# Kernel tuning notes

Measured on AMD Instinct MI355X. Metric: run time of the kernel, lower is better.

Reference implementation:

```python
import jax, jax.numpy as jnp
import numpy as np

N_HEADS = 8
EPS = 1e-8


def _build_gp_map():
    # Cl(4,1) geometric-product structure constants. Blade index = 5-bit mask,
    # e1..e5 = bits 0..4; metric (+,+,+,+,-): e5 (bit 4) squares to -1.
    def pc(n):
        return bin(n).count("1")
    g = np.zeros((32, 32, 32), np.float32)
    for a in range(32):
        for b in range(32):
            swaps = 0
            aa = a >> 1
            while aa:
                swaps += pc(aa & b)
                aa >>= 1
            sign = -1.0 if (swaps & 1) else 1.0
            if (a & b) & 0b10000:  # shared e5 factor contributes -1
                sign = -sign
            g[a, b, a ^ b] = sign
    return g

GP_MAP = jnp.asarray(_build_gp_map())          # (32,32,32)
BIVEC_IDX = jnp.array([3, 5, 6, 9, 10, 12, 17, 18, 20, 24])  # grade-2 blades
SCALAR_VECTOR_IDX = np.array([0, 1, 2, 4, 8, 16])            # grade-0 + grade-1


def normalize_cl41(x):
    return x / jnp.sqrt(jnp.sum(x * x, axis=-1, keepdims=True) + EPS)


def geometric_linear(w, x):
    # w: (O,I,32), x: (...,I,32) -> (...,O,32)
    wg = jnp.einsum('oij,jlk->oilk', w, GP_MAP)     # fold gp_map into weight
    out = jnp.einsum('oilk,...il->...ok', wg, x)
    return normalize_cl41(out)


def _init_weight(key, out_f, in_f):
    # Grade-aware Xavier: only scalar + vector lanes are nonzero.
    std = 1.0 / np.sqrt(in_f * 32)
    vals = jax.random.normal(key, (out_f, in_f, len(SCALAR_VECTOR_IDX)), jnp.float32) * std
    w = jnp.zeros((out_f, in_f, 32), jnp.float32)
    return w.at[:, :, SCALAR_VECTOR_IDX].set(vals)


def setup_inputs() -> dict:
    key = jax.random.key(0)
    kx, kq, kk, kv, ko = jax.random.split(key, 5)
    B, S, D = 2, 384, 128
    x = jax.random.normal(kx, (B, S, D, 32), jnp.float32)
    return {
        'x': x,
        'wq': _init_weight(kq, D, D),
        'wk': _init_weight(kk, D, D),
        'wv': _init_weight(kv, D, D),
        'wo': _init_weight(ko, D, D),
        'attn_lambda': jnp.float32(0.1),
    }


def reference(x, wq, wk, wv, wo, attn_lambda):
    B, S, D, _ = x.shape
    H = N_HEADS
    hd = D // H
    def split_heads(t):  # (B,S,D,32) -> (B,H,S,hd,32)
        return t.reshape(B, S, H, hd, 32).transpose(0, 2, 1, 3, 4)
    q = split_heads(geometric_linear(wq, x))
    k = split_heads(geometric_linear(wk, x))
    v = split_heads(geometric_linear(wv, x))

    # Geometric product Q*K contracted over head_dim, then over gp_map lanes.
    qg = jnp.einsum('bhsdi,ijk->bhsdjk', q, GP_MAP)      # (B,H,S,hd,32,32)
    raw_mv = jnp.einsum('bhsdjk,bhxdj->bhsxk', qg, k)    # (B,H,S,S,32)
    raw_mv = normalize_cl41(raw_mv)

    scalar_part = raw_mv[..., 0]
    biv = raw_mv[..., BIVEC_IDX]
    bivector_norm = jnp.sqrt(jnp.sum(biv * biv, axis=-1) + EPS)
    score = (scalar_part + attn_lambda * bivector_norm) / np.sqrt(hd).astype(np.float32)
    attn_probs = jax.nn.softmax(score, axis=-1)          # (B,H,S,S)

    out = jnp.einsum('bhsx,bhxdl->bhsdl', attn_probs, v)  # (B,H,S,hd,32)
    out = out.transpose(0, 2, 1, 3, 4).reshape(B, S, D, 32)
    return geometric_linear(wo, out)
```

## Files before the change

kernel.cpp:

```cpp
#include <hip/hip_runtime.h>
#include <math.h>

#define BB    2
#define SS    384
#define DD    128
#define NH    8
#define HDIM  16
#define NBH   16
#define BS    768

typedef unsigned int   u32;
typedef unsigned short u16;
typedef __attribute__((ext_vector_type(8))) short short8;
typedef __attribute__((ext_vector_type(4))) float f32x4;

struct SignTab { float v[32][32]; };
constexpr int popcnt32c(int x){ int c=0; for(int i=0;i<32;i++) c += (x>>i)&1; return c; }
constexpr int signgp_int(int a, int b){
  int swaps=0; int aa=a>>1;
  while(aa){ swaps += popcnt32c(aa & b); aa >>= 1; }
  int s = (swaps & 1) ? -1 : 1;
  if ((a & b) & 16) s = -s;
  return s;
}
constexpr SignTab make_signs(){
  SignTab t{};
  for(int a=0;a<32;a++) for(int b=0;b<32;b++)
    t.v[a][b] = (float)signgp_int(a,b);
  return t;
}
constexpr SignTab GPS = make_signs();

struct MaskTab { u32 v[4][8][4][4]; };
constexpr MaskTab mkmask(){
  MaskTab t{};
  for(int w=0;w<4;w++) for(int u=0;u<8;u++) for(int q=0;q<4;q++) for(int r=0;r<4;r++){
    u32 m = 0;
    for(int h=0;h<2;h++){
      int j = 2*r + h;
      int i = (q<<3) | j;
      int c = (w<<3) | u;
      if (signgp_int(i, i^c) < 0) m |= (h ? 0x80000000u : 0x8000u);
    }
    t.v[w][u][q][r] = m;
  }
  return t;
}
constexpr MaskTab MT = mkmask();

__device__ __forceinline__ u16 f2bf(float f){
  u32 x = __float_as_uint(f);
  return (u16)((x + 0x7FFFu + ((x>>16)&1u)) >> 16);
}
__device__ __forceinline__ float bf2f(u16 h){
  return __uint_as_float(((u32)h) << 16);
}

#define XLS 33
__global__ __launch_bounds__(256) void gather_k(const float* __restrict__ src,
                                                u16* __restrict__ xg,
                                                const float* __restrict__ wq,
                                                const float* __restrict__ wk,
                                                const float* __restrict__ wv,
                                                const float* __restrict__ wo,
                                                u16* __restrict__ wpk2){
  if (blockIdx.y == 1){
    int idx = blockIdx.x*256 + threadIdx.x;
    int o   = idx / 768;
    int rem = idx - o*768;
    int jp  = rem >> 7;
    int i   = rem & 127;
    const int SV[6] = {0,1,2,4,8,16};
    const float* ww[4] = {wq, wk, wv, wo};
    #pragma unroll
    for(int p=0;p<4;p++)
      wpk2[p*98304 + idx] = f2bf(ww[p][(o*128 + i)*32 + SV[jp]]);
    return;
  }

  __shared__ float xl[2*128*XLS];
  int t = threadIdx.x;
  int bs0 = blockIdx.x*2;
  int bsl = t >> 7, i = t & 127;

  float row[32];
  const float4* s4 = (const float4*)(src + (((size_t)(bs0+bsl)*128 + i)*32));
  #pragma unroll
  for(int r=0;r<8;r++){
    float4 v = s4[r];
    row[r*4+0]=v.x; row[r*4+1]=v.y; row[r*4+2]=v.z; row[r*4+3]=v.w;
  }
  float* xrow = xl + bsl*128*XLS + i*XLS;
  #pragma unroll
  for(int l=0;l<32;l++) xrow[l] = row[l];
  __syncthreads();

  const int SV[6] = {0,1,2,4,8,16};
  u32* xg32 = (u32*)xg;
  #pragma unroll 4
  for(int r=0;r<96;r++){
    int wr = t + r*256;
    int k   = wr / 768;
    int rem = wr - k*768;
    int bl  = rem / 384;
    int r2  = rem - bl*384;
    int jp  = r2 >> 6;
    int ip  = r2 & 63;
    int i2  = ip*2;
    int b   = SV[jp] ^ k;
    float sg = GPS.v[SV[jp]][b];
    const float* base = xl + bl*128*XLS;
    float f0 = base[ i2   *XLS + b] * sg;
    float f1 = base[(i2+1)*XLS + b] * sg;
    u32 pk = (u32)f2bf(f0) | ((u32)f2bf(f1) << 16);
    xg32[((size_t)k*768 + bs0 + bl)*384 + jp*64 + ip] = pk;
  }
}

#define LSTR 40
__global__ __launch_bounds__(256) void gemm_proj(const u16* __restrict__ xg,
                                                 const u16* __restrict__ wpkA,
                                                 u16* __restrict__ tmpA){
  __shared__ __align__(16) u16 As[128*LSTR];
  __shared__ __align__(16) u16 Bs[128*LSTR];
  int t = threadIdx.x;
  int Mt = blockIdx.x, k = blockIdx.y, p = blockIdx.z;
  const u16* wpk = wpkA + (size_t)p*98304;
  u16* tmp = tmpA + (size_t)p*32*768*128;

  int w = t >> 6, lane = t & 63;
  int q = lane >> 4, n16 = lane & 15;
  int wm = w >> 1, wn = w & 1;

  f32x4 acc[4][4];
  #pragma unroll
  for(int a=0;a<4;a++)
    #pragma unroll
    for(int b=0;b<4;b++) acc[a][b] = (f32x4){0.f,0.f,0.f,0.f};

  int r0 = t>>2, c0 = (t&3)*8;
  int r1 = (t+256)>>2, c1 = ((t+256)&3)*8;
  const u16* Aab = xg + ((size_t)k*768 + Mt*128)*768;

  uint4 pa0, pa1, pb0, pb1;
  {
    pa0 = *(const uint4*)(Aab + (size_t)r0*768 + c0);
    pa1 = *(const uint4*)(Aab + (size_t)r1*768 + c1);
    pb0 = *(const uint4*)(wpk + (size_t)r0*768 + c0);
    pb1 = *(const uint4*)(wpk + (size_t)r1*768 + c1);
  }

  for(int kt=0; kt<24; kt++){
    __syncthreads();
    *(uint4*)(As + r0*LSTR + c0) = pa0;
    *(uint4*)(As + r1*LSTR + c1) = pa1;
    *(uint4*)(Bs + r0*LSTR + c0) = pb0;
    *(uint4*)(Bs + r1*LSTR + c1) = pb1;
    __syncthreads();
    if (kt < 23){
      int kn = (kt+1)*32;
      pa0 = *(const uint4*)(Aab + (size_t)r0*768 + kn + c0);
      pa1 = *(const uint4*)(Aab + (size_t)r1*768 + kn + c1);
      pb0 = *(const uint4*)(wpk + (size_t)r0*768 + kn + c0);
      pb1 = *(const uint4*)(wpk + (size_t)r1*768 + kn + c1);
    }
    short8 a[4], b[4];
    #pragma unroll
    for(int mi=0;mi<4;mi++)
      a[mi] = *(const short8*)(As + (wm*64 + mi*16 + n16)*LSTR + q*8);
    #pragma unroll
    for(int ni=0;ni<4;ni++)
      b[ni] = *(const short8*)(Bs + (wn*64 + ni*16 + n16)*LSTR + q*8);
    #pragma unroll
    for(int mi=0;mi<4;mi++)
      #pragma unroll
      for(int ni=0;ni<4;ni++)
        acc[mi][ni] = __builtin_amdgcn_mfma_f32_16x16x32_bf16(a[mi], b[ni], acc[mi][ni], 0,0,0);
  }

  #pragma unroll
  for(int mi=0;mi<4;mi++){
    #pragma unroll
    for(int r=0;r<4;r++){
      int m = Mt*128 + wm*64 + mi*16 + q*4 + r;
      #pragma unroll
      for(int ni=0;ni<4;ni++){
        int n = wn*64 + ni*16 + n16;
        tmp[((size_t)k*768 + m)*128 + n] = f2bf(acc[mi][ni][r]);
      }
    }
  }
}

__global__ __launch_bounds__(256) void norm3(const u16* __restrict__ tmpA,
                                             u16* __restrict__ qhb,
                                             u16* __restrict__ khb,
                                             u16* __restrict__ vbb){
  int z = blockIdx.y;
  const u16* tmp = tmpA + (size_t)z*32*768*128;
  u16* dst = (z==0)?qhb:(z==1)?khb:vbb;
  int t = threadIdx.x;
  int bsl = t >> 7, o = t & 127;
  int bs = blockIdx.x*2 + bsl;

  float a[32];
  float ssum = 1e-8f;
  #pragma unroll
  for(int k=0;k<32;k++){
    a[k] = bf2f(tmp[((size_t)k*768 + bs)*128 + o]);
    ssum = fmaf(a[k], a[k], ssum);
  }
  float inv = 1.0f / sqrtf(ssum);

  int b = bs / SS, s = bs - b*SS;
  int h = o >> 4, d = o & 15;
  uint4* og4 = (uint4*)(dst + (((size_t)(b*NH + h)*SS + s)*512 + d*32));
  #pragma unroll
  for(int l=0;l<4;l++){
    uint4 v;
    v.x = (u32)f2bf(a[8*l+0]*inv) | ((u32)f2bf(a[8*l+1]*inv)<<16);
    v.y = (u32)f2bf(a[8*l+2]*inv) | ((u32)f2bf(a[8*l+3]*inv)<<16);
    v.z = (u32)f2bf(a[8*l+4]*inv) | ((u32)f2bf(a[8*l+5]*inv)<<16);
    v.w = (u32)f2bf(a[8*l+6]*inv) | ((u32)f2bf(a[8*l+7]*inv)<<16);
    og4[l] = v;
  }
}

__global__ __launch_bounds__(256) void norm_out(const u16* __restrict__ tmp,
                                                float* __restrict__ dst){
  int t = threadIdx.x;
  int bsl = t >> 7, o = t & 127;
  int bs = blockIdx.x*2 + bsl;

  float a[32];
  float ssum = 1e-8f;
  #pragma unroll
  for(int k=0;k<32;k++){
    a[k] = bf2f(tmp[((size_t)k*768 + bs)*128 + o]);
    ssum = fmaf(a[k], a[k], ssum);
  }
  float inv = 1.0f / sqrtf(ssum);
  float4* og = (float4*)(dst + ((size_t)bs*128 + o)*32);
  #pragma unroll
  for(int l4=0;l4<8;l4++){
    float4 v;
    v.x = a[4*l4+0]*inv; v.y = a[4*l4+1]*inv;
    v.z = a[4*l4+2]*inv; v.w = a[4*l4+3]*inv;
    og[l4] = v;
  }
}

#define TVS 528
__global__ __launch_bounds__(256) void transpose_v(const u16* __restrict__ vb,
                                                   u16* __restrict__ vt){
  __shared__ __align__(16) u16 vl[32*TVS];
  int t = threadIdx.x;
  int xt = blockIdx.x, bh = blockIdx.y;
  const u16* src = vb + ((size_t)bh*SS + xt*32)*512;
  #pragma unroll
  for(int j=0;j<8;j++){
    int f = t + j*256; int row = f>>6, c = (f&63)*8;
    *(uint4*)(vl + row*TVS + c) = *(const uint4*)(src + (size_t)row*512 + c);
  }
  __syncthreads();
  u16* dst = vt + (size_t)bh*512*SS + xt*32;
  #pragma unroll
  for(int j=0;j<8;j++){
    int f = t + j*256; int dl = f>>2, c4 = (f&3)*8;
    u16 tmp[8];
    #pragma unroll
    for(int e=0;e<8;e++) tmp[e] = vl[(c4+e)*TVS + dl];
    *(uint4*)(dst + (size_t)dl*SS + c4) = *(uint4*)tmp;
  }
}

#define QSTR 264
__global__ __launch_bounds__(256,2) void scores_mfma(const u16* __restrict__ qh,
                                                     const u16* __restrict__ kh,
                                                     float* __restrict__ sc,
                                                     const float* __restrict__ lam){
  __shared__ __align__(16) u16 smem[(64+16)*QSTR];
  u16* qs = smem;
  u16* ks = smem + 64*QSTR;
  int t = threadIdx.x;
  int id  = blockIdx.x;
  int xcd = id & 7;
  int g   = id >> 3;
  int half= g / 144;
  int r9  = g - half*144;
  int bh  = xcd + 8*half;
  int st  = r9 / 24;
  int xt  = r9 - st*24;

  u32 hsh  = (u32)id * 0x9E3779B9u;
  int rot  = (int)(hsh >> 29);
  int hrot = (int)(hsh >> 28) & 1;

  int w = t >> 6, lane = t & 63, q = lane >> 4, mn = lane & 15;
  float lm = lam[0];

  u32 FM[8][4];
  #pragma unroll
  for(int u=0;u<8;u++)
    #pragma unroll
    for(int r=0;r<4;r++) FM[u][r] = MT.v[w][u][q][r];

  f32x4 acc[4][8];
  #pragma unroll
  for(int mi=0;mi<4;mi++)
    #pragma unroll
    for(int u=0;u<8;u++) acc[mi][u] = (f32x4){0.f,0.f,0.f,0.f};

  for(int hi=0; hi<2; hi++){
    int h = hi ^ hrot;
    __syncthreads();
    const u16* qbase = qh + ((size_t)bh*SS + st*64)*512 + h*256;
    const u16* kbase = kh + ((size_t)bh*SS + xt*16)*512 + h*256;
    #pragma unroll
    for(int j=0;j<8;j++){
      int f = t + j*256;
      int row = f>>5, c = (f&31)*8;
      *(uint4*)(qs + row*QSTR + c) = *(const uint4*)(qbase + (size_t)row*512 + c);
    }
    #pragma unroll
    for(int j=0;j<2;j++){
      int f = t + j*256;
      int row = f>>5, c = (f&31)*8;
      *(uint4*)(ks + row*QSTR + c) = *(const uint4*)(kbase + (size_t)row*512 + c);
    }
    __syncthreads();

    for(int ktl=0; ktl<8; ktl++){
      int ke = (ktl + rot) & 7;
      short8 a[4];
      #pragma unroll
      for(int mi=0;mi<4;mi++)
        a[mi] = *(const short8*)(qs + (mi*16+mn)*QSTR + ke*32 + q*8);
      uint4 khd = *(const uint4*)(ks + mn*QSTR + ke*32 + ((q^w)<<3));
      u32 kk[4]  = {khd.x, khd.y, khd.z, khd.w};
      u32 kks[4];
      #pragma unroll
      for(int r=0;r<4;r++) kks[r] = (kk[r]>>16)|(kk[r]<<16);
      #pragma unroll
      for(int u=0;u<8;u++){
        union { u32 w32[4]; short8 s; } bf;
        #pragma unroll
        for(int r=0;r<4;r++){
          u32 v = (u & 1) ? kks[r ^ (u>>1)] : kk[r ^ (u>>1)];
          bf.w32[r] = v ^ FM[u][r];
        }
        #pragma unroll
        for(int mi=0;mi<4;mi++)
          acc[mi][u] = __builtin_amdgcn_mfma_f32_16x16x32_bf16(a[mi], bf.s, acc[mi][u], 0, 0, 0);
      }
    }
  }
  __syncthreads();

  float* pss = (float*)smem;
  float* pbb = pss + 64*68;
  float* ps0 = pbb + 64*68;

  #pragma unroll
  for(int mi=0;mi<4;mi++){
    #pragma unroll
    for(int rr=0;rr<4;rr++){
      float ssv = 0.f, bbv = 0.f;
      #pragma unroll
      for(int u=0;u<8;u++){
        int c = w*8 + u;
        bool isb = (c==3)||(c==5)||(c==6)||(c==9)||(c==10)||(c==12)||
                   (c==17)||(c==18)||(c==20)||(c==24);
        float v = acc[mi][u][rr];
        ssv = fmaf(v, v, ssv);
        if (isb) bbv = fmaf(v, v, bbv);
      }
      int s = mi*16 + q*4 + rr;
      pss[s*68 + w*16 + mn] = ssv;
      pbb[s*68 + w*16 + mn] = bbv;
      if (w == 0) ps0[s*17 + mn] = acc[mi][0][rr];
    }
  }
  __syncthreads();

  int x = t & 15, s0 = t >> 4;
  #pragma unroll
  for(int ssi=0; ssi<4; ssi++){
    int s = s0 + ssi*16;
    float ss = 1e-8f, bb = 0.f;
    #pragma unroll
    for(int ww=0; ww<4; ww++){
      ss += pss[s*68 + ww*16 + x];
      bb += pbb[s*68 + ww*16 + x];
    }
    float inv = 1.0f / sqrtf(ss);
    float s0v = ps0[s*17+x];
    float score = (s0v*inv + lm*sqrtf(bb*inv*inv + 1e-8f)) * 0.25f;
    sc[((size_t)bh*SS + st*64 + s)*SS + xt*16 + x] = score;
  }
}

#define PBS 392
#define VSS 40
__global__ __launch_bounds__(256,2) void pv_mfma(const float* __restrict__ sc,
                                                 const u16* __restrict__ vt,
                                                 u32* __restrict__ xgo){
  __shared__ __align__(16) u16 pb[16*PBS];
  __shared__ __align__(16) u16 vsm[256*VSS];
  int t = threadIdx.x;
  int id  = blockIdx.x;
  int xcd = id & 7;
  int rest= id >> 3;
  int z   = rest & 1;
  int g2  = rest >> 1;
  int half= g2 / 24;
  int st  = g2 - half*24;
  int bh  = xcd + 8*half;
  int w = t >> 6, lane = t & 63, q = lane >> 4, mn = lane & 15;

  u32 hsh = (u32)id * 0x9E3779B9u;
  int rotp = (int)(hsh >> 30) * 3;

  {
    int row = t >> 4, gg = t & 15;
    const float* srow = sc + ((size_t)bh*SS + st*16 + row)*SS;
    float v[24];
    float mx = -1e30f;
    #pragma unroll
    for(int k2=0;k2<24;k2++){ v[k2] = srow[gg + k2*16]; mx = fmaxf(mx, v[k2]); }
    #pragma unroll
    for(int off=8; off; off>>=1) mx = fmaxf(mx, __shfl_xor(mx, off));
    float sum = 0.f;
    #pragma unroll
    for(int k2=0;k2<24;k2++){ v[k2] = __expf(v[k2]-mx); sum += v[k2]; }
    #pragma unroll
    for(int off=8; off; off>>=1) sum += __shfl_xor(sum, off);
    float inv = 1.f/sum;
    #pragma unroll
    for(int k2=0;k2<24;k2++) pb[row*PBS + gg + k2*16] = f2bf(v[k2]*inv);
  }

  f32x4 acc[4];
  #pragma unroll
  for(int mt=0;mt<4;mt++) acc[mt] = (f32x4){0.f,0.f,0.f,0.f};

  const u16* vtb = vt + (size_t)bh*512*SS + (size_t)z*256*SS;
  for(int kt=0; kt<12; kt++){
    int ke = kt + rotp; if (ke >= 12) ke -= 12;
    __syncthreads();
    #pragma unroll
    for(int j=0;j<4;j++){
      int f = t + j*256;
      int dl = f>>2, c4 = (f&3)*8;
      *(uint4*)(vsm + dl*VSS + c4) = *(const uint4*)(vtb + (size_t)dl*SS + ke*32 + c4);
    }
    __syncthreads();
    short8 b = *(const short8*)(pb + mn*PBS + ke*32 + q*8);
    #pragma unroll
    for(int mt=0;mt<4;mt++){
      short8 a = *(const short8*)(vsm + ((w*4+mt)*16 + mn)*VSS + q*8);
      acc[mt] = __builtin_amdgcn_mfma_f32_16x16x32_bf16(a, b, acc[mt], 0, 0, 0);
    }
  }
  __syncthreads();

  float* ot = (float*)vsm;
  #pragma unroll
  for(int mt=0;mt<4;mt++)
    #pragma unroll
    for(int rr=0;rr<4;rr++){
      int dl = (w*4+mt)*16 + q*4 + rr;
      int row = ((dl & 31) << 3) | (dl >> 5);
      ot[row*17 + mn] = acc[mt][rr];
    }
  __syncthreads();

  int b = bh >> 3, h = bh & 7;
  int bs_base = b*SS + st*16;
  const int SVc[6] = {0,1,2,4,8,16};
  #pragma unroll 4
  for(int it=0; it<48; it++){
    int idx = it*256 + t;
    int dpl = idx & 3;
    int s   = (idx >> 2) & 15;
    int jl  = idx >> 6;
    int jp  = jl >> 5;
    int l   = jl & 31;
    int k   = SVc[jp] ^ l;
    float sg = GPS.v[SVc[jp]][l];
    float v0 = sg * ot[(l*8 + dpl*2    )*17 + s];
    float v1 = sg * ot[(l*8 + dpl*2 + 1)*17 + s];
    u32 pk = (u32)f2bf(v0) | ((u32)f2bf(v1) << 16);
    xgo[((size_t)k*768 + bs_base + s)*384 + (size_t)(jp*64 + h*8 + z*4 + dpl)] = pk;
  }
}

extern "C" void kernel_launch(void* const* d_in, const int* in_sizes, int n_in,
                              void* d_out, int out_size, void* d_ws, size_t ws_size,
                              hipStream_t stream) {
  const float* x   = (const float*)d_in[0];
  const float* wq  = (const float*)d_in[1];
  const float* wk  = (const float*)d_in[2];
  const float* wv  = (const float*)d_in[3];
  const float* wo  = (const float*)d_in[4];
  const float* lam = (const float*)d_in[5];
  float* out = (float*)d_out;

  char* ws = (char*)d_ws;
  size_t off = 0;
  u16*   wpk2 = (u16*)(ws + off); off += (size_t)4*98304*2;
  u16*   xg   = (u16*)(ws + off); off += (size_t)32*768*768*2;
  u16*   tmp3 = (u16*)(ws + off); off += (size_t)3*32*768*128*2;
  u16*   vt   = tmp3;
  float* sc   = (float*)((char*)tmp3 + 6291456);
  u16*   qhb  = (u16*)(ws + off); off += (size_t)NBH*SS*512*2;
  u16*   khb  = (u16*)(ws + off); off += (size_t)NBH*SS*512*2;
  u16*   vb   = (u16*)(ws + off); off += (size_t)NBH*SS*512*2;

  gather_k<<<dim3(384,2),256,0,stream>>>(x, xg, wq, wk, wv, wo, wpk2);
  gemm_proj<<<dim3(6,32,3),256,0,stream>>>(xg, wpk2, tmp3);
  norm3<<<dim3(384,3),256,0,stream>>>(tmp3, qhb, khb, vb);
  transpose_v<<<dim3(12,16),256,0,stream>>>(vb, vt);

  scores_mfma<<<2304,256,0,stream>>>(qhb, khb, sc, lam);
  pv_mfma<<<768,256,0,stream>>>(sc, vt, (u32*)xg);

  gemm_proj<<<dim3(6,32,1),256,0,stream>>>(xg, wpk2 + (size_t)3*98304, tmp3);
  norm_out<<<384,256,0,stream>>>(tmp3, out);
}
```

Before: 256.5 us.

## Replace expanded gathered GP operand with compact transposed x and on-the-fly sign masks

Instead of materializing a 32x-expanded, sign-applied gathered activation buffer (32*768*768 bf16), the input and attention output are stored once as a lane-major bf16 transpose. The projection GEMM now computes the XOR-permuted blade source per K-tile and flips bf16 sign bits with a precomputed mask while loading. This removes a large write-then-read of the expanded buffer in both the input and output projections. The cost is extra address and XOR work in the GEMM load path, and the A loads are now strided across blade slices.

```diff
diff --git a/kernel.cpp b/kernel.cpp
--- a/kernel.cpp
+++ b/kernel.cpp
@@ -48,6 +48,16 @@
 }
 constexpr MaskTab MT = mkmask();
 
+struct PMask { u32 v[6][32]; };
+constexpr PMask mkpmask(){
+  PMask t{};
+  const int SV[6] = {0,1,2,4,8,16};
+  for(int jp=0;jp<6;jp++) for(int k=0;k<32;k++)
+    t.v[jp][k] = (signgp_int(SV[jp], SV[jp]^k) < 0) ? 0x80008000u : 0u;
+  return t;
+}
+constexpr PMask PM = mkpmask();
+
 __device__ __forceinline__ u16 f2bf(float f){
   u32 x = __float_as_uint(f);
   return (u16)((x + 0x7FFFu + ((x>>16)&1u)) >> 16);
@@ -56,14 +66,13 @@
   return __uint_as_float(((u32)h) << 16);
 }
 
-#define XLS 33
-__global__ __launch_bounds__(256) void gather_k(const float* __restrict__ src,
-                                                u16* __restrict__ xg,
-                                                const float* __restrict__ wq,
-                                                const float* __restrict__ wk,
-                                                const float* __restrict__ wv,
-                                                const float* __restrict__ wo,
-                                                u16* __restrict__ wpk2){
+__global__ __launch_bounds__(256) void transpose_x(const float* __restrict__ src,
+                                                   u16* __restrict__ xT,
+                                                   const float* __restrict__ wq,
+                                                   const float* __restrict__ wk,
+                                                   const float* __restrict__ wv,
+                                                   const float* __restrict__ wo,
+                                                   u16* __restrict__ wpk2){
   if (blockIdx.y == 1){
     int idx = blockIdx.x*256 + threadIdx.x;
     int o   = idx / 768;
@@ -78,55 +87,44 @@
     return;
   }
 
-  __shared__ float xl[2*128*XLS];
-  int t = threadIdx.x;
-  int bs0 = blockIdx.x*2;
-  int bsl = t >> 7, i = t & 127;
-
-  float row[32];
-  const float4* s4 = (const float4*)(src + (((size_t)(bs0+bsl)*128 + i)*32));
-  #pragma unroll
-  for(int r=0;r<8;r++){
-    float4 v = s4[r];
-    row[r*4+0]=v.x; row[r*4+1]=v.y; row[r*4+2]=v.z; row[r*4+3]=v.w;
-  }
-  float* xrow = xl + bsl*128*XLS + i*XLS;
-  #pragma unroll
-  for(int l=0;l<32;l++) xrow[l] = row[l];
+  __shared__ __align__(16) u16 xb[32*264];
+  int t = threadIdx.x;
+  int r0 = blockIdx.x*256;
+
+  const float4* s4 = (const float4*)(src + (size_t)r0*32);
+  #pragma unroll
+  for(int j=0;j<8;j++){
+    int f = t + j*256;
+    int rr = f >> 3;
+    int bc = (f & 7)*4;
+    float4 v = s4[f];
+    xb[(bc+0)*264 + rr] = f2bf(v.x);
+    xb[(bc+1)*264 + rr] = f2bf(v.y);
+    xb[(bc+2)*264 + rr] = f2bf(v.z);
+    xb[(bc+3)*264 + rr] = f2bf(v.w);
+  }
   __syncthreads();
-
-  const int SV[6] = {0,1,2,4,8,16};
-  u32* xg32 = (u32*)xg;
-  #pragma unroll 4
-  for(int r=0;r<96;r++){
-    int wr = t + r*256;
-    int k   = wr / 768;
-    int rem = wr - k*768;
-    int bl  = rem / 384;
-    int r2  = rem - bl*384;
-    int jp  = r2 >> 6;
-    int ip  = r2 & 63;
-    int i2  = ip*2;
-    int b   = SV[jp] ^ k;
-    float sg = GPS.v[SV[jp]][b];
-    const float* base = xl + bl*128*XLS;
-    float f0 = base[ i2   *XLS + b] * sg;
-    float f1 = base[(i2+1)*XLS + b] * sg;
-    u32 pk = (u32)f2bf(f0) | ((u32)f2bf(f1) << 16);
-    xg32[((size_t)k*768 + bs0 + bl)*384 + jp*64 + ip] = pk;
+  #pragma unroll
+  for(int j=0;j<4;j++){
+    int f = t + j*256;
+    int b = f >> 5;
+    int ch = f & 31;
+    uint4 v = *(const uint4*)(xb + b*264 + ch*8);
+    *(uint4*)(xT + (size_t)b*98304 + r0 + ch*8) = v;
   }
 }
 
 #define LSTR 40
-__global__ __launch_bounds__(256) void gemm_proj(const u16* __restrict__ xg,
+__global__ __launch_bounds__(256) void gemm_proj(const u16* __restrict__ Asrc,
                                                  const u16* __restrict__ wpkA,
-                                                 u16* __restrict__ tmpA){
+                                                 u16* __restrict__ tmpA,
+                                                 int poff){
   __shared__ __align__(16) u16 As[128*LSTR];
   __shared__ __align__(16) u16 Bs[128*LSTR];
   int t = threadIdx.x;
-  int Mt = blockIdx.x, k = blockIdx.y, p = blockIdx.z;
-  const u16* wpk = wpkA + (size_t)p*98304;
-  u16* tmp = tmpA + (size_t)p*32*768*128;
+  int Mt = blockIdx.x, k = blockIdx.y;
+  const u16* wpk = wpkA + (size_t)(poff + blockIdx.z)*98304;
+  u16* tmp = tmpA + (size_t)blockIdx.z*32*768*128;
 
   int w = t >> 6, lane = t & 63;
   int q = lane >> 4, n16 = lane & 15;
@@ -140,12 +138,19 @@
 
   int r0 = t>>2, c0 = (t&3)*8;
   int r1 = (t+256)>>2, c1 = ((t+256)&3)*8;
-  const u16* Aab = xg + ((size_t)k*768 + Mt*128)*768;
+
+  const int SV[6] = {0,1,2,4,8,16};
+  #define APTR(kt_) (Asrc + ((size_t)(SV[(kt_)>>2]^k)*768 + Mt*128)*128 + ((kt_)&3)*32)
+  #define AMSK(kt_) (PM.v[(kt_)>>2][k])
 
   uint4 pa0, pa1, pb0, pb1;
   {
-    pa0 = *(const uint4*)(Aab + (size_t)r0*768 + c0);
-    pa1 = *(const uint4*)(Aab + (size_t)r1*768 + c1);
+    const u16* ap = APTR(0);
+    u32 am = AMSK(0);
+    pa0 = *(const uint4*)(ap + (size_t)r0*128 + c0);
+    pa1 = *(const uint4*)(ap + (size_t)r1*128 + c1);
+    pa0.x ^= am; pa0.y ^= am; pa0.z ^= am; pa0.w ^= am;
+    pa1.x ^= am; pa1.y ^= am; pa1.z ^= am; pa1.w ^= am;
     pb0 = *(const uint4*)(wpk + (size_t)r0*768 + c0);
     pb1 = *(const uint4*)(wpk + (size_t)r1*768 + c1);
   }
@@ -159,8 +164,12 @@
     __syncthreads();
     if (kt < 23){
       int kn = (kt+1)*32;
-      pa0 = *(const uint4*)(Aab + (size_t)r0*768 + kn + c0);
-      pa1 = *(const uint4*)(Aab + (size_t)r1*768 + kn + c1);
+      const u16* ap = APTR(kt+1);
+      u32 am = AMSK(kt+1);
+      pa0 = *(const uint4*)(ap + (size_t)r0*128 + c0);
+      pa1 = *(const uint4*)(ap + (size_t)r1*128 + c1);
+      pa0.x ^= am; pa0.y ^= am; pa0.z ^= am; pa0.w ^= am;
+      pa1.x ^= am; pa1.y ^= am; pa1.z ^= am; pa1.w ^= am;
       pb0 = *(const uint4*)(wpk + (size_t)r0*768 + kn + c0);
       pb1 = *(const uint4*)(wpk + (size_t)r1*768 + kn + c1);
     }
@@ -177,6 +186,8 @@
       for(int ni=0;ni<4;ni++)
         acc[mi][ni] = __builtin_amdgcn_mfma_f32_16x16x32_bf16(a[mi], b[ni], acc[mi][ni], 0,0,0);
   }
+  #undef APTR
+  #undef AMSK
 
   #pragma unroll
   for(int mi=0;mi<4;mi++){
@@ -404,7 +415,7 @@
 #define VSS 40
 __global__ __launch_bounds__(256,2) void pv_mfma(const float* __restrict__ sc,
                                                  const u16* __restrict__ vt,
-                                                 u32* __restrict__ xgo){
+                                                 u16* __restrict__ omT){
   __shared__ __align__(16) u16 pb[16*PBS];
   __shared__ __align__(16) u16 vsm[256*VSS];
   int t = threadIdx.x;
@@ -477,21 +488,15 @@
 
   int b = bh >> 3, h = bh & 7;
   int bs_base = b*SS + st*16;
-  const int SVc[6] = {0,1,2,4,8,16};
-  #pragma unroll 4
-  for(int it=0; it<48; it++){
-    int idx = it*256 + t;
-    int dpl = idx & 3;
-    int s   = (idx >> 2) & 15;
-    int jl  = idx >> 6;
-    int jp  = jl >> 5;
-    int l   = jl & 31;
-    int k   = SVc[jp] ^ l;
-    float sg = GPS.v[SVc[jp]][l];
-    float v0 = sg * ot[(l*8 + dpl*2    )*17 + s];
-    float v1 = sg * ot[(l*8 + dpl*2 + 1)*17 + s];
-    u32 pk = (u32)f2bf(v0) | ((u32)f2bf(v1) << 16);
-    xgo[((size_t)k*768 + bs_base + s)*384 + (size_t)(jp*64 + h*8 + z*4 + dpl)] = pk;
+  #pragma unroll
+  for(int j=0;j<2;j++){
+    int idx = t + j*256;
+    int s = idx & 15;
+    int l = idx >> 4;
+    u16 t8[8];
+    #pragma unroll
+    for(int e=0;e<8;e++) t8[e] = f2bf(ot[(l*8+e)*17 + s]);
+    *(uint4*)(omT + ((size_t)l*768 + bs_base + s)*128 + h*16 + z*8) = *(uint4*)t8;
   }
 }
 
@@ -509,7 +514,8 @@
   char* ws = (char*)d_ws;
   size_t off = 0;
   u16*   wpk2 = (u16*)(ws + off); off += (size_t)4*98304*2;
-  u16*   xg   = (u16*)(ws + off); off += (size_t)32*768*768*2;
+  u16*   xT   = (u16*)(ws + off); off += (size_t)32*98304*2;
+  u16*   omT  = xT;
   u16*   tmp3 = (u16*)(ws + off); off += (size_t)3*32*768*128*2;
   u16*   vt   = tmp3;
   float* sc   = (float*)((char*)tmp3 + 6291456);
@@ -517,14 +523,14 @@
   u16*   khb  = (u16*)(ws + off); off += (size_t)NBH*SS*512*2;
   u16*   vb   = (u16*)(ws + off); off += (size_t)NBH*SS*512*2;
 
-  gather_k<<<dim3(384,2),256,0,stream>>>(x, xg, wq, wk, wv, wo, wpk2);
-  gemm_proj<<<dim3(6,32,3),256,0,stream>>>(xg, wpk2, tmp3);
+  transpose_x<<<dim3(384,2),256,0,stream>>>(x, xT, wq, wk, wv, wo, wpk2);
+  gemm_proj<<<dim3(6,32,3),256,0,stream>>>(xT, wpk2, tmp3, 0);
   norm3<<<dim3(384,3),256,0,stream>>>(tmp3, qhb, khb, vb);
   transpose_v<<<dim3(12,16),256,0,stream>>>(vb, vt);
 
   scores_mfma<<<2304,256,0,stream>>>(qhb, khb, sc, lam);
-  pv_mfma<<<768,256,0,stream>>>(sc, vt, (u32*)xg);
-
-  gemm_proj<<<dim3(6,32,1),256,0,stream>>>(xg, wpk2 + (size_t)3*98304, tmp3);
+  pv_mfma<<<768,256,0,stream>>>(sc, vt, omT);
+
+  gemm_proj<<<dim3(6,32,1),256,0,stream>>>(omT, wpk2, tmp3, 3);
   norm_out<<<384,256,0,stream>>>(tmp3, out);
 }
```

New measurement: 224.7 us. 12.4% less time.
